# Kernel optimization log

Hardware: AMD Instinct MI355X
Metric: run time of the kernel (lower is better)

Reference implementation:

```python
import jax, jax.numpy as jnp
import numpy as np

N = 100000
E = 1600000
IN = 256
H = 4
F = 64
NEG_SLOPE = 0.05


def setup_inputs() -> dict:
    key = jax.random.key(0)
    ks = jax.random.split(key, 8)
    feat = jax.random.normal(ks[0], (N, IN), dtype=jnp.float32)
    src = jax.random.randint(ks[1], (E,), 0, N, dtype=jnp.int64)
    dst = jax.random.randint(ks[2], (E,), 0, N, dtype=jnp.int64)
    W_fc = jax.random.normal(ks[3], (H * F, IN), dtype=jnp.float32) * (2.0 / np.sqrt(IN + H * F))
    attn_l = jax.random.normal(ks[4], (H, F), dtype=jnp.float32) * 0.1
    attn_r = jax.random.normal(ks[5], (H, F), dtype=jnp.float32) * 0.1
    W_res = jax.random.normal(ks[6], (H * F, IN), dtype=jnp.float32) * (2.0 / np.sqrt(IN + H * F))
    bias = jnp.zeros((H * F,), dtype=jnp.float32)
    return {"feat": feat, "src": src, "dst": dst, "W_fc": W_fc,
            "attn_l": attn_l, "attn_r": attn_r, "W_res": W_res, "bias": bias}


def _leaky_relu(x):
    return jnp.where(x > 0, x, NEG_SLOPE * x)


def reference(feat, src, dst, W_fc, attn_l, attn_r, W_res, bias):
    # project: [N, H, F]
    feat_src = (feat @ W_fc.T).reshape(N, H, F)
    # attention logits per node: el/er [N, H]
    el = jnp.einsum('nhf,hf->nh', feat_src, attn_l)
    er = jnp.einsum('nhf,hf->nh', feat_src, attn_r)
    # edge SDDMM (u_add_v) + leaky_relu: [E, H]
    e = _leaky_relu(el[src] + er[dst])
    # edge softmax grouped by destination node
    emax = jax.ops.segment_max(e, dst, num_segments=N)          # [N, H]
    emax = jnp.where(jnp.isfinite(emax), emax, 0.0)             # empty segments
    ex = jnp.exp(e - emax[dst])                                 # [E, H]
    esum = jax.ops.segment_sum(ex, dst, num_segments=N)         # [N, H]
    a = ex / jnp.maximum(esum[dst], 1e-20)                      # [E, H]
    # u_mul_e + sum aggregation (SpMM): [N, H, F]
    msgs = feat_src[src] * a[:, :, None]                        # [E, H, F]
    rst = jax.ops.segment_sum(msgs, dst, num_segments=N)
    # residual + bias
    rst = rst + (feat @ W_res.T).reshape(N, H, F)
    rst = rst + bias.reshape(1, H, F)
    return rst, a
```

## Files before the change

### kernel.cpp

```cpp
#include <hip/hip_runtime.h>

#define NNODES 100000
#define NEDGES 1600000
#define KDIM 256
#define CDIM 256
#define NHEAD 4
#define FDIM 64
#define NEG 0.05f

typedef short bf16x8 __attribute__((ext_vector_type(8)));
typedef float f32x4  __attribute__((ext_vector_type(4)));
typedef __attribute__((address_space(3))) void*       lds_vp;
typedef __attribute__((address_space(1))) const void* glb_cvp;

__device__ __forceinline__ unsigned short f2b(float x) {
    unsigned int u = __float_as_uint(x);
    return (unsigned short)((u + 0x7FFFu + ((u >> 16) & 1u)) >> 16);
}
__device__ __forceinline__ float b2f(unsigned short b) {
    return __uint_as_float(((unsigned int)b) << 16);
}
__device__ __forceinline__ float lrelu(float x) { return x > 0.f ? x : NEG * x; }

__global__ __launch_bounds__(256) void cvt_feat(const float* __restrict__ in,
                                                unsigned short* __restrict__ out)
{
    int i = (blockIdx.x * 256 + threadIdx.x) * 4;
    float4 v = *(const float4*)(in + i);
    ushort4 o;
    o.x = f2b(v.x); o.y = f2b(v.y); o.z = f2b(v.z); o.w = f2b(v.w);
    *(ushort4*)(out + i) = o;
}

__global__ __launch_bounds__(256) void cvt_w(const float* __restrict__ Wfc,
                                             const float* __restrict__ Wres,
                                             unsigned short* __restrict__ out)
{
    int i = (blockIdx.x * 256 + threadIdx.x) * 4;
    float4 v = (i < 65536) ? *(const float4*)(Wfc + i)
                           : *(const float4*)(Wres + (i - 65536));
    ushort4 o;
    o.x = f2b(v.x); o.y = f2b(v.y); o.z = f2b(v.z); o.w = f2b(v.w);
    *(ushort4*)(out + i) = o;
}

__global__ __launch_bounds__(256) void gemm_mfma(
    const unsigned short* __restrict__ featb,
    const unsigned short* __restrict__ Wb,
    const float* __restrict__ bias,
    unsigned short* __restrict__ fsb,
    float* __restrict__ rst)
{
    __shared__ __align__(16) char smem[32768];
    char* sA = smem;
    char* sB = smem + 16384;

    const int tid = threadIdx.x;
    const int w = tid >> 6, l = tid & 63;
    const int wm = w & 1, wn = w >> 1;
    const int row0 = blockIdx.x * 128;
    const int ny = blockIdx.y;

    f32x4 acc[4][4];
#pragma unroll
    for (int tm = 0; tm < 4; ++tm)
#pragma unroll
        for (int tn = 0; tn < 4; ++tn) acc[tm][tn] = (f32x4)0.f;

    const int srow = tid >> 3;
    const int sslot = tid & 7;

    for (int k0 = 0; k0 < 256; k0 += 64) {
        if (k0) __syncthreads();
#pragma unroll
        for (int it = 0; it < 4; ++it) {
            int r = srow + it * 32;
            int gr = row0 + r; if (gr >= NNODES) gr = NNODES - 1;
            int kc = sslot ^ (r & 7);
            const unsigned short* g = featb + (size_t)gr * 256 + k0 + kc * 8;
            void* sp = sA + (it * 256 + w * 64) * 16;
            __builtin_amdgcn_global_load_lds((glb_cvp)g, (lds_vp)sp, 16, 0, 0);
        }
#pragma unroll
        for (int it = 0; it < 4; ++it) {
            int r = srow + it * 32;
            int kc = sslot ^ (r & 7);
            const unsigned short* g = Wb + (size_t)(ny * 128 + r) * 256 + k0 + kc * 8;
            void* sp = sB + (it * 256 + w * 64) * 16;
            __builtin_amdgcn_global_load_lds((glb_cvp)g, (lds_vp)sp, 16, 0, 0);
        }
        __syncthreads();

        const int quad = l >> 4;
#pragma unroll
        for (int kk = 0; kk < 2; ++kk) {
            const int kc = kk * 4 + quad;
            bf16x8 af[4], bq[4];
#pragma unroll
            for (int tm = 0; tm < 4; ++tm) {
                int m = wm * 64 + tm * 16 + (l & 15);
                af[tm] = *(const bf16x8*)(sA + m * 128 + ((kc ^ (m & 7)) * 16));
            }
#pragma unroll
            for (int tn = 0; tn < 4; ++tn) {
                int n = wn * 64 + tn * 16 + (l & 15);
                bq[tn] = *(const bf16x8*)(sB + n * 128 + ((kc ^ (n & 7)) * 16));
            }
#pragma unroll
            for (int tm = 0; tm < 4; ++tm)
#pragma unroll
                for (int tn = 0; tn < 4; ++tn)
                    acc[tm][tn] = __builtin_amdgcn_mfma_f32_16x16x32_bf16(
                        af[tm], bq[tn], acc[tm][tn], 0, 0, 0);
        }
    }

    const int quad = l >> 4, c15 = l & 15;
    if (ny < 2) {
#pragma unroll
        for (int tm = 0; tm < 4; ++tm) {
            int rb = row0 + wm * 64 + tm * 16 + quad * 4;
#pragma unroll
            for (int tn = 0; tn < 4; ++tn) {
                int cg = ny * 128 + wn * 64 + tn * 16 + c15;
#pragma unroll
                for (int reg = 0; reg < 4; ++reg) {
                    int r = rb + reg;
                    if (r < NNODES) fsb[(size_t)r * 256 + cg] = f2b(acc[tm][tn][reg]);
                }
            }
        }
    } else {
#pragma unroll
        for (int tm = 0; tm < 4; ++tm) {
            int rb = row0 + wm * 64 + tm * 16 + quad * 4;
#pragma unroll
            for (int tn = 0; tn < 4; ++tn) {
                int co = (ny - 2) * 128 + wn * 64 + tn * 16 + c15;
                float b = bias[co];
#pragma unroll
                for (int reg = 0; reg < 4; ++reg) {
                    int r = rb + reg;
                    if (r < NNODES) rst[(size_t)r * 256 + co] = acc[tm][tn][reg] + b;
                }
            }
        }
    }
}

__global__ __launch_bounds__(256) void eler_kernel(
    const unsigned short* __restrict__ fsb,
    const float* __restrict__ attn_l, const float* __restrict__ attn_r,
    float* __restrict__ el, float* __restrict__ er)
{
    const int tid = threadIdx.x;
    const int wv = tid >> 6, lane = tid & 63;
    const int n = blockIdx.x * 4 + wv;
    const int c0 = lane * 4;

    ushort4 v = *(const ushort4*)(fsb + (size_t)n * 256 + c0);
    float4 al = *(const float4*)(attn_l + c0);
    float4 ar = *(const float4*)(attn_r + c0);
    float f0 = b2f(v.x), f1 = b2f(v.y), f2 = b2f(v.z), f3 = b2f(v.w);
    float pl = f0 * al.x + f1 * al.y + f2 * al.z + f3 * al.w;
    float pr = f0 * ar.x + f1 * ar.y + f2 * ar.z + f3 * ar.w;
#pragma unroll
    for (int d = 1; d < 16; d <<= 1) {
        pl += __shfl_xor(pl, d);
        pr += __shfl_xor(pr, d);
    }
    if ((lane & 15) == 0) {
        int h = lane >> 4;
        el[n * NHEAD + h] = pl;
        er[n * NHEAD + h] = pr;
    }
}

__global__ __launch_bounds__(256) void count_kernel(const int* __restrict__ dst,
                                                    int* __restrict__ cnt)
{
    int e = blockIdx.x * 256 + threadIdx.x;
    if (e < NEDGES) atomicAdd(&cnt[dst[e]], 1);
}

__global__ __launch_bounds__(256) void offset_kernel(const int* __restrict__ cnt,
                                                     int* __restrict__ off,
                                                     int* __restrict__ cursor,
                                                     int* __restrict__ total)
{
    int n = blockIdx.x * 256 + threadIdx.x;
    if (n < NNODES) {
        int c = cnt[n];
        int o = atomicAdd(total, c);
        off[n] = o;
        cursor[n] = o;
    }
}

__global__ __launch_bounds__(256) void scatter_kernel(const int* __restrict__ dst,
                                                      int* __restrict__ cursor,
                                                      int* __restrict__ perm)
{
    int e = blockIdx.x * 256 + threadIdx.x;
    if (e < NEDGES) {
        int p = atomicAdd(&cursor[dst[e]], 1);
        perm[p] = e;
    }
}

__global__ __launch_bounds__(256) void agg_kernel(
    const int* __restrict__ src, const int* __restrict__ perm,
    const int* __restrict__ off, const int* __restrict__ cnt,
    const float* __restrict__ el, const float* __restrict__ er,
    const unsigned short* __restrict__ fsb,
    float* __restrict__ rst,
    float* __restrict__ m_arr, float* __restrict__ inv_arr)
{
    const int tid = threadIdx.x;
    const int wv = tid >> 6, lane = tid & 63;
    const int n = blockIdx.x * 4 + wv;
    const int deg = cnt[n];
    if (deg == 0) return;
    const int o0 = off[n];
    const int h = lane >> 4;

    const float4 er4 = *(const float4*)(er + (size_t)n * NHEAD);

    float4 m = make_float4(-1e30f, -1e30f, -1e30f, -1e30f);
    float4 s = make_float4(0.f, 0.f, 0.f, 0.f);
    int s0_save = 0; float4 l0_save = m;

    for (int base = 0; base < deg; base += 64) {
        int i = base + lane;
        bool valid = i < deg;
        int e = perm[o0 + (valid ? i : deg - 1)];
        int sidx = src[e];
        float4 ev = *(const float4*)(el + (size_t)sidx * NHEAD);
        float4 l;
        l.x = lrelu(ev.x + er4.x); l.y = lrelu(ev.y + er4.y);
        l.z = lrelu(ev.z + er4.z); l.w = lrelu(ev.w + er4.w);
        if (base == 0) { s0_save = sidx; l0_save = l; }
        float mn;
        mn = fmaxf(m.x, l.x); s.x = s.x * __expf(m.x - mn) + (valid ? __expf(l.x - mn) : 0.f); m.x = mn;
        mn = fmaxf(m.y, l.y); s.y = s.y * __expf(m.y - mn) + (valid ? __expf(l.y - mn) : 0.f); m.y = mn;
        mn = fmaxf(m.z, l.z); s.z = s.z * __expf(m.z - mn) + (valid ? __expf(l.z - mn) : 0.f); m.z = mn;
        mn = fmaxf(m.w, l.w); s.w = s.w * __expf(m.w - mn) + (valid ? __expf(l.w - mn) : 0.f); m.w = mn;
    }
#pragma unroll
    for (int d = 32; d > 0; d >>= 1) {
        float mo, so, mn;
        mo = __shfl_xor(m.x, d); so = __shfl_xor(s.x, d);
        mn = fmaxf(m.x, mo); s.x = s.x * __expf(m.x - mn) + so * __expf(mo - mn); m.x = mn;
        mo = __shfl_xor(m.y, d); so = __shfl_xor(s.y, d);
        mn = fmaxf(m.y, mo); s.y = s.y * __expf(m.y - mn) + so * __expf(mo - mn); m.y = mn;
        mo = __shfl_xor(m.z, d); so = __shfl_xor(s.z, d);
        mn = fmaxf(m.z, mo); s.z = s.z * __expf(m.z - mn) + so * __expf(mo - mn); m.z = mn;
        mo = __shfl_xor(m.w, d); so = __shfl_xor(s.w, d);
        mn = fmaxf(m.w, mo); s.w = s.w * __expf(m.w - mn) + so * __expf(mo - mn); m.w = mn;
    }
    float4 inv;
    inv.x = 1.f / fmaxf(s.x, 1e-20f);
    inv.y = 1.f / fmaxf(s.y, 1e-20f);
    inv.z = 1.f / fmaxf(s.z, 1e-20f);
    inv.w = 1.f / fmaxf(s.w, 1e-20f);
    if (lane == 0) {
        *(float4*)(m_arr + (size_t)n * NHEAD) = m;
        *(float4*)(inv_arr + (size_t)n * NHEAD) = inv;
    }

    float4 acc = make_float4(0.f, 0.f, 0.f, 0.f);
    for (int base = 0; base < deg; base += 64) {
        int i = base + lane;
        bool valid = i < deg;
        int sidx; float4 l;
        if (base == 0) { sidx = s0_save; l = l0_save; }
        else {
            int e = perm[o0 + (valid ? i : deg - 1)];
            sidx = src[e];
            float4 ev = *(const float4*)(el + (size_t)sidx * NHEAD);
            l.x = lrelu(ev.x + er4.x); l.y = lrelu(ev.y + er4.y);
            l.z = lrelu(ev.z + er4.z); l.w = lrelu(ev.w + er4.w);
        }
        float4 a;
        a.x = valid ? __expf(l.x - m.x) * inv.x : 0.f;
        a.y = valid ? __expf(l.y - m.y) * inv.y : 0.f;
        a.z = valid ? __expf(l.z - m.z) * inv.z : 0.f;
        a.w = valid ? __expf(l.w - m.w) * inv.w : 0.f;

        int nc = min(64, deg - base);
        for (int j = 0; j < nc; ++j) {
            int sj = __shfl(sidx, j);
            float ax = __shfl(a.x, j), ay = __shfl(a.y, j);
            float az = __shfl(a.z, j), aw = __shfl(a.w, j);
            float av = (h == 0) ? ax : (h == 1) ? ay : (h == 2) ? az : aw;
            uint2 p = *(const uint2*)(fsb + (size_t)sj * 256 + lane * 4);
            acc.x = fmaf(av, __uint_as_float(p.x << 16), acc.x);
            acc.y = fmaf(av, __uint_as_float(p.x & 0xffff0000u), acc.y);
            acc.z = fmaf(av, __uint_as_float(p.y << 16), acc.z);
            acc.w = fmaf(av, __uint_as_float(p.y & 0xffff0000u), acc.w);
        }
    }
    size_t ro = (size_t)n * 256 + lane * 4;
    float4 r = *(float4*)(rst + ro);
    r.x += acc.x; r.y += acc.y; r.z += acc.z; r.w += acc.w;
    *(float4*)(rst + ro) = r;
}

__global__ __launch_bounds__(256) void aout_kernel(
    const int* __restrict__ src, const int* __restrict__ dst,
    const float* __restrict__ el, const float* __restrict__ er,
    const float* __restrict__ m_arr, const float* __restrict__ inv_arr,
    float* __restrict__ a_out)
{
    int e = blockIdx.x * 256 + threadIdx.x;
    if (e >= NEDGES) return;
    int sidx = src[e], d = dst[e];
    float4 ev = *(const float4*)(el + (size_t)sidx * NHEAD);
    float4 rv = *(const float4*)(er + (size_t)d * NHEAD);
    float4 m4 = *(const float4*)(m_arr + (size_t)d * NHEAD);
    float4 i4 = *(const float4*)(inv_arr + (size_t)d * NHEAD);
    float4 a;
    a.x = __expf(lrelu(ev.x + rv.x) - m4.x) * i4.x;
    a.y = __expf(lrelu(ev.y + rv.y) - m4.y) * i4.y;
    a.z = __expf(lrelu(ev.z + rv.z) - m4.z) * i4.z;
    a.w = __expf(lrelu(ev.w + rv.w) - m4.w) * i4.w;
    *(float4*)(a_out + (size_t)e * NHEAD) = a;
}

extern "C" void kernel_launch(void* const* d_in, const int* in_sizes, int n_in,
                              void* d_out, int out_size, void* d_ws, size_t ws_size,
                              hipStream_t stream) {
    const float* feat   = (const float*)d_in[0];
    const int*   src    = (const int*)d_in[1];
    const int*   dst    = (const int*)d_in[2];
    const float* Wfc    = (const float*)d_in[3];
    const float* attn_l = (const float*)d_in[4];
    const float* attn_r = (const float*)d_in[5];
    const float* Wres   = (const float*)d_in[6];
    const float* bias   = (const float*)d_in[7];

    float* rst   = (float*)d_out;
    float* a_out = (float*)d_out + (size_t)NNODES * CDIM;

    unsigned short* featb = (unsigned short*)d_ws;
    unsigned short* fsb   = featb + (size_t)NNODES * CDIM;
    unsigned short* Wb    = fsb + (size_t)NNODES * CDIM;
    float* el      = (float*)(Wb + 512 * 256);
    float* er      = el + (size_t)NNODES * NHEAD;
    float* m_arr   = er + (size_t)NNODES * NHEAD;
    float* inv_arr = m_arr + (size_t)NNODES * NHEAD;
    int* cnt    = (int*)(inv_arr + (size_t)NNODES * NHEAD);
    int* off    = cnt + NNODES;
    int* cursor = off + NNODES;
    int* total  = cursor + NNODES;
    int* perm   = total + 4;

    hipMemsetAsync(cnt, 0, NNODES * sizeof(int), stream);
    hipMemsetAsync(total, 0, 4 * sizeof(int), stream);

    cvt_feat<<<(NNODES * CDIM) / (256 * 4), 256, 0, stream>>>(feat, featb);
    cvt_w<<<(512 * 256) / (256 * 4), 256, 0, stream>>>(Wfc, Wres, Wb);

    dim3 ggrid((NNODES + 127) / 128, 4);
    gemm_mfma<<<ggrid, 256, 0, stream>>>(featb, Wb, bias, fsb, rst);

    eler_kernel<<<NNODES / 4, 256, 0, stream>>>(fsb, attn_l, attn_r, el, er);

    count_kernel<<<(NEDGES + 255) / 256, 256, 0, stream>>>(dst, cnt);
    offset_kernel<<<(NNODES + 255) / 256, 256, 0, stream>>>(cnt, off, cursor, total);
    scatter_kernel<<<(NEDGES + 255) / 256, 256, 0, stream>>>(dst, cursor, perm);

    agg_kernel<<<NNODES / 4, 256, 0, stream>>>(src, perm, off, cnt, el, er,
                                               fsb, rst, m_arr, inv_arr);
    aout_kernel<<<(NEDGES + 255) / 256, 256, 0, stream>>>(src, dst, el, er,
                                                          m_arr, inv_arr, a_out);
}
```

Before: 741.4 us.

## Swizzle GEMM block order and stage attention weights in LDS for aggregation

The GEMM launch becomes a 1D grid remapped so each group of 8 row tiles is processed across all 4 column tiles together, so the same feature rows are reused from L2 while still resident. The aggregation inner loop stops broadcasting the source index and four attention values via five shuffles per edge. Instead it writes them to per-wave LDS, reads them back with a scalar readfirstlane index, and unrolls the loop by 4. This trades cross-lane shuffles for LDS traffic and adds padded early-exit blocks in the GEMM grid.

```diff
diff --git a/kernel.cpp b/kernel.cpp
--- a/kernel.cpp
+++ b/kernel.cpp
@@ -51,6 +51,12 @@
     unsigned short* __restrict__ fsb,
     float* __restrict__ rst)
 {
+    const int b = blockIdx.x;
+    const int grp = b >> 5, w32 = b & 31;
+    const int bx = grp * 8 + (w32 & 7);
+    const int ny = w32 >> 3;
+    if (bx >= (NNODES + 127) / 128) return;
+
     __shared__ __align__(16) char smem[32768];
     char* sA = smem;
     char* sB = smem + 16384;
@@ -58,8 +64,7 @@
     const int tid = threadIdx.x;
     const int w = tid >> 6, l = tid & 63;
     const int wm = w & 1, wn = w >> 1;
-    const int row0 = blockIdx.x * 128;
-    const int ny = blockIdx.y;
+    const int row0 = bx * 128;
 
     f32x4 acc[4][4];
 #pragma unroll
@@ -137,11 +142,11 @@
 #pragma unroll
             for (int tn = 0; tn < 4; ++tn) {
                 int co = (ny - 2) * 128 + wn * 64 + tn * 16 + c15;
-                float b = bias[co];
+                float b2 = bias[co];
 #pragma unroll
                 for (int reg = 0; reg < 4; ++reg) {
                     int r = rb + reg;
-                    if (r < NNODES) rst[(size_t)r * 256 + co] = acc[tm][tn][reg] + b;
+                    if (r < NNODES) rst[(size_t)r * 256 + co] = acc[tm][tn][reg] + b2;
                 }
             }
         }
@@ -223,6 +228,11 @@
     if (deg == 0) return;
     const int o0 = off[n];
     const int h = lane >> 4;
+
+    __shared__ __align__(16) float a_sh[4][64][4];
+    __shared__ int s_sh[4][64];
+    float* aw = &a_sh[wv][0][0];
+    int*   sw = &s_sh[wv][0];
 
     const float4 er4 = *(const float4*)(er + (size_t)n * NHEAD);
 
@@ -269,6 +279,7 @@
     }
 
     float4 acc = make_float4(0.f, 0.f, 0.f, 0.f);
+    const int laneoff = lane << 2;
     for (int base = 0; base < deg; base += 64) {
         int i = base + lane;
         bool valid = i < deg;
@@ -286,21 +297,23 @@
         a.y = valid ? __expf(l.y - m.y) * inv.y : 0.f;
         a.z = valid ? __expf(l.z - m.z) * inv.z : 0.f;
         a.w = valid ? __expf(l.w - m.w) * inv.w : 0.f;
+        *(float4*)(aw + (lane << 2)) = a;
+        sw[lane] = sidx;
 
         int nc = min(64, deg - base);
+#pragma unroll 4
         for (int j = 0; j < nc; ++j) {
-            int sj = __shfl(sidx, j);
-            float ax = __shfl(a.x, j), ay = __shfl(a.y, j);
-            float az = __shfl(a.z, j), aw = __shfl(a.w, j);
-            float av = (h == 0) ? ax : (h == 1) ? ay : (h == 2) ? az : aw;
-            uint2 p = *(const uint2*)(fsb + (size_t)sj * 256 + lane * 4);
+            float av = aw[(j << 2) + h];
+            int sj = __builtin_amdgcn_readfirstlane(sw[j]);
+            const unsigned short* rp = fsb + ((size_t)sj << 8) + laneoff;
+            uint2 p = *(const uint2*)rp;
             acc.x = fmaf(av, __uint_as_float(p.x << 16), acc.x);
             acc.y = fmaf(av, __uint_as_float(p.x & 0xffff0000u), acc.y);
             acc.z = fmaf(av, __uint_as_float(p.y << 16), acc.z);
             acc.w = fmaf(av, __uint_as_float(p.y & 0xffff0000u), acc.w);
         }
     }
-    size_t ro = (size_t)n * 256 + lane * 4;
+    size_t ro = (size_t)n * 256 + (lane << 2);
     float4 r = *(float4*)(rst + ro);
     r.x += acc.x; r.y += acc.y; r.z += acc.z; r.w += acc.w;
     *(float4*)(rst + ro) = r;
@@ -361,8 +374,7 @@
     cvt_feat<<<(NNODES * CDIM) / (256 * 4), 256, 0, stream>>>(feat, featb);
     cvt_w<<<(512 * 256) / (256 * 4), 256, 0, stream>>>(Wfc, Wres, Wb);
 
-    dim3 ggrid((NNODES + 127) / 128, 4);
-    gemm_mfma<<<ggrid, 256, 0, stream>>>(featb, Wb, bias, fsb, rst);
+    gemm_mfma<<<3136, 256, 0, stream>>>(featb, Wb, bias, fsb, rst);
 
     eler_kernel<<<NNODES / 4, 256, 0, stream>>>(fsb, attn_l, attn_r, el, er);
 
```

Measured after the change: 724.6 us. 1.02x faster.
